# Kernel optimization log

Hardware: AMD Instinct MI355X
Metric: run time of the kernel (lower is better)

Reference implementation:

```python
import jax, jax.numpy as jnp
import numpy as np

B, C, H, W = 8, 256, 64, 64
NUM_HEADS = 4


def setup_inputs() -> dict:
    key = jax.random.key(0)
    ks = jax.random.split(key, 6)
    s = 0.02  # small init scale for 1x1 conv weights
    return {
        "x": jax.random.normal(ks[0], (B, C, H, W), jnp.float32),
        "cproj": jax.random.normal(ks[1], (B, C, H, W), jnp.float32),
        "wq": jax.random.normal(ks[2], (C, C), jnp.float32) * s,
        "bq": jnp.zeros((C,), jnp.float32),
        "wkv": jax.random.normal(ks[3], (2 * C, C), jnp.float32) * s,
        "bkv": jnp.zeros((2 * C,), jnp.float32),
        "wo": jax.random.normal(ks[4], (C, C), jnp.float32) * s,  # zero_module in torch; random here for a meaningful baseline
        "bo": jnp.zeros((C,), jnp.float32),
    }


def reference(x, cproj, wq, bq, wkv, bkv, wo, bo):
    Bb, Cc, Hh, Ww = x.shape
    N = Hh * Ww
    h = NUM_HEADS
    d = Cc // h
    scale = 1.0 / jnp.sqrt(jnp.sqrt(jnp.asarray(Cc, jnp.float32)))

    xf = x.reshape(Bb, Cc, N)
    cf = cproj.reshape(Bb, Cc, N)

    # 1x1 convs == channel matmuls
    Q = jnp.einsum('oc,bcn->bon', wq, xf) + bq[None, :, None]           # (B,C,N)
    KV = jnp.einsum('oc,bcn->bon', wkv, cf) + bkv[None, :, None]        # (B,2C,N)
    K, V = KV[:, :Cc], KV[:, Cc:]

    # softmax over channel-dim-within-head for q, over spatial N for k
    q = jax.nn.softmax(Q.reshape(Bb, h, d, N) * scale, axis=2).reshape(Bb, Cc, N)
    k = jax.nn.softmax(K.reshape(Bb, h, d, N), axis=3).reshape(Bb, Cc, N)

    # linear-attention: (B,C,C) context, then project back to N — note heads are mixed, per original bmm
    context = jnp.einsum('bcn,bdn->bcd', k, V)
    out = jnp.einsum('bcd,bdn->bcn', context, q)

    out = jnp.einsum('oc,bcn->bon', wo, out) + bo[None, :, None]
    return out.reshape(Bb, Cc, Hh, Ww)
```

## Files before the change

kernel.cpp:

```cpp
#include <hip/hip_runtime.h>

#define B_ 8
#define C_ 256
#define N_ 4096
#define H_ 4
#define KVC_ 512
#define NSPLIT 8

typedef float f32x4 __attribute__((ext_vector_type(4)));
typedef __bf16 bf16x8 __attribute__((ext_vector_type(8)));
typedef unsigned short u16x8 __attribute__((ext_vector_type(8)));
typedef unsigned short u16x4 __attribute__((ext_vector_type(4)));

union BU8 { u16x8 u; bf16x8 b; };

__device__ __forceinline__ unsigned short f2bf(float f) {
  unsigned u = __float_as_uint(f);
  u += 0x7fff + ((u >> 16) & 1);
  return (unsigned short)(u >> 16);
}

__device__ __forceinline__ f32x4 mfma16(bf16x8 a, bf16x8 b, f32x4 c) {
  return __builtin_amdgcn_mfma_f32_16x16x32_bf16(a, b, c, 0, 0, 0);
}

__global__ __launch_bounds__(256) void qproj_softmax(
    const float* __restrict__ wq, const float* __restrict__ x,
    const float* __restrict__ bq, unsigned short* __restrict__ qT) {
  __shared__ unsigned short As[256][40];
  __shared__ unsigned short Bs[32][68];
  __shared__ float bql[C_];
  const int b = blockIdx.z;
  const int n0 = blockIdx.x * 64;
  const int tid = threadIdx.x;
  const int lane = tid & 63, w = tid >> 6;
  const float* xb = x + (size_t)b * C_ * N_;

  bql[tid] = bq[tid];

  f32x4 acc[16];
#pragma unroll
  for (int i = 0; i < 16; i++) acc[i] = (f32x4){0.f, 0.f, 0.f, 0.f};

  const int colL = lane & 15, kq = lane >> 4;
  for (int kc = 0; kc < C_; kc += 32) {
    __syncthreads();
#pragma unroll
    for (int i = 0; i < 8; i++) {
      int r = i * 32 + (tid >> 3), c = (tid & 7) * 4;
      float4 v = *(const float4*)&wq[r * C_ + kc + c];
      *(u16x4*)&As[r][c] = (u16x4){f2bf(v.x), f2bf(v.y), f2bf(v.z), f2bf(v.w)};
    }
#pragma unroll
    for (int i = 0; i < 2; i++) {
      int r = i * 16 + (tid >> 4), c = (tid & 15) * 4;
      float4 v = *(const float4*)&xb[(size_t)(kc + r) * N_ + n0 + c];
      *(u16x4*)&Bs[r][c] = (u16x4){f2bf(v.x), f2bf(v.y), f2bf(v.z), f2bf(v.w)};
    }
    __syncthreads();

    BU8 bu;
#pragma unroll
    for (int j = 0; j < 8; j++) bu.u[j] = Bs[kq * 8 + j][w * 16 + colL];
    bf16x8 bf = bu.b;
#pragma unroll
    for (int mt = 0; mt < 16; mt++) {
      bf16x8 af = *(const bf16x8*)&As[mt * 16 + colL][kq * 8];
      acc[mt] = mfma16(af, bf, acc[mt]);
    }
  }

  const int quad = lane >> 4;
  const int n = n0 + w * 16 + colL;
  unsigned short* qbase = qT + ((size_t)b * N_ + n) * C_;
#pragma unroll
  for (int h = 0; h < H_; h++) {
    float v[16];
    float mx = -1e30f;
#pragma unroll
    for (int i = 0; i < 4; i++) {
      int mt = 4 * h + i;
#pragma unroll
      for (int r = 0; r < 4; r++) {
        int m = mt * 16 + quad * 4 + r;
        float val = (acc[mt][r] + bql[m]) * 0.25f;
        v[i * 4 + r] = val;
        mx = fmaxf(mx, val);
      }
    }
    mx = fmaxf(mx, __shfl_xor(mx, 16));
    mx = fmaxf(mx, __shfl_xor(mx, 32));
    float s = 0.f;
#pragma unroll
    for (int j = 0; j < 16; j++) { v[j] = __expf(v[j] - mx); s += v[j]; }
    s += __shfl_xor(s, 16);
    s += __shfl_xor(s, 32);
    float inv = 1.0f / s;
#pragma unroll
    for (int i = 0; i < 4; i++) {
      u16x4 o = (u16x4){f2bf(v[i * 4 + 0] * inv), f2bf(v[i * 4 + 1] * inv),
                        f2bf(v[i * 4 + 2] * inv), f2bf(v[i * 4 + 3] * inv)};
      *(u16x4*)(qbase + (4 * h + i) * 16 + quad * 4) = o;
    }
  }
}

__global__ __launch_bounds__(256) void kvproj(
    const float* __restrict__ wkv, const float* __restrict__ cp,
    const float* __restrict__ bkv, float* __restrict__ Kf,
    unsigned short* __restrict__ Vb) {
  __shared__ unsigned short As[128][40];
  __shared__ unsigned short Bs[32][136];
  const int b = blockIdx.z;
  const int m0 = blockIdx.y * 128, n0 = blockIdx.x * 128;
  const int tid = threadIdx.x, lane = tid & 63, w = tid >> 6;
  const int m0w = (w >> 1) * 64, n0w = (w & 1) * 64;
  const int colL = lane & 15, kq = lane >> 4;
  const float* cpb = cp + (size_t)b * C_ * N_;

  f32x4 acc[4][4];
#pragma unroll
  for (int i = 0; i < 4; i++)
#pragma unroll
    for (int j = 0; j < 4; j++) acc[i][j] = (f32x4){0.f, 0.f, 0.f, 0.f};

  for (int kc = 0; kc < C_; kc += 32) {
    __syncthreads();
#pragma unroll
    for (int i = 0; i < 4; i++) {
      int r = i * 32 + (tid >> 3), c = (tid & 7) * 4;
      float4 v = *(const float4*)&wkv[(size_t)(m0 + r) * C_ + kc + c];
      *(u16x4*)&As[r][c] = (u16x4){f2bf(v.x), f2bf(v.y), f2bf(v.z), f2bf(v.w)};
    }
#pragma unroll
    for (int i = 0; i < 4; i++) {
      int r = i * 8 + (tid >> 5), c = (tid & 31) * 4;
      float4 v = *(const float4*)&cpb[(size_t)(kc + r) * N_ + n0 + c];
      *(u16x4*)&Bs[r][c] = (u16x4){f2bf(v.x), f2bf(v.y), f2bf(v.z), f2bf(v.w)};
    }
    __syncthreads();

    bf16x8 bfr[4];
#pragma unroll
    for (int nt = 0; nt < 4; nt++) {
      BU8 bu;
#pragma unroll
      for (int j = 0; j < 8; j++) bu.u[j] = Bs[kq * 8 + j][n0w + nt * 16 + colL];
      bfr[nt] = bu.b;
    }
#pragma unroll
    for (int mt = 0; mt < 4; mt++) {
      bf16x8 af = *(const bf16x8*)&As[m0w + mt * 16 + colL][kq * 8];
#pragma unroll
      for (int nt = 0; nt < 4; nt++) acc[mt][nt] = mfma16(af, bfr[nt], acc[mt][nt]);
    }
  }

  const int quad = lane >> 4;
#pragma unroll
  for (int mt = 0; mt < 4; mt++) {
#pragma unroll
    for (int r = 0; r < 4; r++) {
      int m = m0 + m0w + mt * 16 + quad * 4 + r;
      float bias = bkv[m];
#pragma unroll
      for (int nt = 0; nt < 4; nt++) {
        int n = n0 + n0w + nt * 16 + colL;
        float val = acc[mt][nt][r] + bias;
        if (m0 < C_) {
          Kf[((size_t)b * C_ + m) * N_ + n] = val;
        } else {
          Vb[((size_t)b * C_ + (m - C_)) * N_ + n] = f2bf(val);
        }
      }
    }
  }
}

__global__ __launch_bounds__(256) void ksoftmax(const float* __restrict__ Kf,
                                                unsigned short* __restrict__ kb) {
  const int b = blockIdx.x >> 8, c = blockIdx.x & 255;
  const float* row = Kf + ((size_t)b * C_ + c) * N_;
  unsigned short* orow = kb + ((size_t)b * C_ + c) * N_;
  const int t = threadIdx.x, lane = t & 63, wv = t >> 6;
  __shared__ float red[8];

  float4 v[4];
  float mx = -1e30f;
#pragma unroll
  for (int i = 0; i < 4; i++) {
    v[i] = *(const float4*)&row[i * 1024 + t * 4];
    mx = fmaxf(fmaxf(fmaxf(mx, v[i].x), fmaxf(v[i].y, v[i].z)), v[i].w);
  }
#pragma unroll
  for (int o = 32; o > 0; o >>= 1) mx = fmaxf(mx, __shfl_down(mx, o));
  if (lane == 0) red[wv] = mx;
  __syncthreads();
  mx = fmaxf(fmaxf(red[0], red[1]), fmaxf(red[2], red[3]));

  float s = 0.f;
#pragma unroll
  for (int i = 0; i < 4; i++) {
    v[i].x = __expf(v[i].x - mx); v[i].y = __expf(v[i].y - mx);
    v[i].z = __expf(v[i].z - mx); v[i].w = __expf(v[i].w - mx);
    s += v[i].x + v[i].y + v[i].z + v[i].w;
  }
#pragma unroll
  for (int o = 32; o > 0; o >>= 1) s += __shfl_down(s, o);
  if (lane == 0) red[4 + wv] = s;
  __syncthreads();
  float inv = 1.0f / (red[4] + red[5] + red[6] + red[7]);
#pragma unroll
  for (int i = 0; i < 4; i++) {
    u16x4 o = (u16x4){f2bf(v[i].x * inv), f2bf(v[i].y * inv),
                      f2bf(v[i].z * inv), f2bf(v[i].w * inv)};
    *(u16x4*)&orow[i * 1024 + t * 4] = o;
  }
}

__global__ __launch_bounds__(256) void ctx_part(
    const unsigned short* __restrict__ kb, const unsigned short* __restrict__ Vb,
    float* __restrict__ ctxp) {
  __shared__ unsigned short As[128][40];
  __shared__ unsigned short Bs[128][40];
  const int z = blockIdx.z, b = z >> 3, s = z & 7;
  const int m0 = blockIdx.y * 128, n0 = blockIdx.x * 128;
  const int tid = threadIdx.x, lane = tid & 63, w = tid >> 6;
  const int m0w = (w >> 1) * 64, n0w = (w & 1) * 64;
  const int colL = lane & 15, kq = lane >> 4;
  const unsigned short* Ab = kb + (size_t)b * C_ * N_;
  const unsigned short* Bb = Vb + (size_t)b * C_ * N_;

  f32x4 acc[4][4];
#pragma unroll
  for (int i = 0; i < 4; i++)
#pragma unroll
    for (int j = 0; j < 4; j++) acc[i][j] = (f32x4){0.f, 0.f, 0.f, 0.f};

  const int kbeg = s * (N_ / NSPLIT);
  for (int kc = kbeg; kc < kbeg + N_ / NSPLIT; kc += 32) {
    __syncthreads();
#pragma unroll
    for (int i = 0; i < 2; i++) {
      int r = i * 64 + (tid >> 2), c = (tid & 3) * 8;
      *(u16x8*)&As[r][c] = *(const u16x8*)&Ab[(size_t)(m0 + r) * N_ + kc + c];
      *(u16x8*)&Bs[r][c] = *(const u16x8*)&Bb[(size_t)(n0 + r) * N_ + kc + c];
    }
    __syncthreads();

    bf16x8 af[4], bfr[4];
#pragma unroll
    for (int mt = 0; mt < 4; mt++) af[mt] = *(const bf16x8*)&As[m0w + mt * 16 + colL][kq * 8];
#pragma unroll
    for (int nt = 0; nt < 4; nt++) bfr[nt] = *(const bf16x8*)&Bs[n0w + nt * 16 + colL][kq * 8];
#pragma unroll
    for (int mt = 0; mt < 4; mt++)
#pragma unroll
      for (int nt = 0; nt < 4; nt++) acc[mt][nt] = mfma16(af[mt], bfr[nt], acc[mt][nt]);
  }

  float* outp = ctxp + ((size_t)s * B_ + b) * C_ * C_;
  const int quad = lane >> 4;
#pragma unroll
  for (int mt = 0; mt < 4; mt++)
#pragma unroll
    for (int nt = 0; nt < 4; nt++)
#pragma unroll
      for (int r = 0; r < 4; r++) {
        int m = m0 + m0w + mt * 16 + quad * 4 + r;
        int n = n0 + n0w + nt * 16 + colL;
        outp[(size_t)m * C_ + n] = acc[mt][nt][r];
      }
}

__global__ __launch_bounds__(256) void ctx_reduce(const float* __restrict__ ctxp,
                                                  unsigned short* __restrict__ ctxs) {
  const size_t e = ((size_t)blockIdx.x * 256 + threadIdx.x) * 4;
  float4 a = {0.f, 0.f, 0.f, 0.f};
#pragma unroll
  for (int s = 0; s < NSPLIT; s++) {
    float4 v = *(const float4*)&ctxp[(size_t)s * B_ * C_ * C_ + e];
    a.x += v.x; a.y += v.y; a.z += v.z; a.w += v.w;
  }
  *(u16x4*)&ctxs[e] = (u16x4){f2bf(a.x), f2bf(a.y), f2bf(a.z), f2bf(a.w)};
}

__global__ __launch_bounds__(256) void oproj(const float* __restrict__ wo,
                                             const unsigned short* __restrict__ ctxs,
                                             unsigned short* __restrict__ ctx2) {
  __shared__ unsigned short As[128][40];
  __shared__ unsigned short Bs[32][136];
  const int b = blockIdx.z;
  const int m0 = blockIdx.y * 128, n0 = blockIdx.x * 128;
  const int tid = threadIdx.x, lane = tid & 63, w = tid >> 6;
  const int m0w = (w >> 1) * 64, n0w = (w & 1) * 64;
  const int colL = lane & 15, kq = lane >> 4;
  const unsigned short* cb = ctxs + (size_t)b * C_ * C_;

  f32x4 acc[4][4];
#pragma unroll
  for (int i = 0; i < 4; i++)
#pragma unroll
    for (int j = 0; j < 4; j++) acc[i][j] = (f32x4){0.f, 0.f, 0.f, 0.f};

  for (int kc = 0; kc < C_; kc += 32) {
    __syncthreads();
#pragma unroll
    for (int i = 0; i < 4; i++) {
      int r = i * 32 + (tid >> 3), c = (tid & 7) * 4;
      float4 v = *(const float4*)&wo[(size_t)(m0 + r) * C_ + kc + c];
      *(u16x4*)&As[r][c] = (u16x4){f2bf(v.x), f2bf(v.y), f2bf(v.z), f2bf(v.w)};
    }
#pragma unroll
    for (int i = 0; i < 2; i++) {
      int r = i * 16 + (tid >> 4), c = (tid & 15) * 8;
      *(u16x8*)&Bs[r][c] = *(const u16x8*)&cb[(size_t)(kc + r) * C_ + n0 + c];
    }
    __syncthreads();

    bf16x8 bfr[4];
#pragma unroll
    for (int nt = 0; nt < 4; nt++) {
      BU8 bu;
#pragma unroll
      for (int j = 0; j < 8; j++) bu.u[j] = Bs[kq * 8 + j][n0w + nt * 16 + colL];
      bfr[nt] = bu.b;
    }
#pragma unroll
    for (int mt = 0; mt < 4; mt++) {
      bf16x8 af = *(const bf16x8*)&As[m0w + mt * 16 + colL][kq * 8];
#pragma unroll
      for (int nt = 0; nt < 4; nt++) acc[mt][nt] = mfma16(af, bfr[nt], acc[mt][nt]);
    }
  }

  unsigned short* ob = ctx2 + (size_t)b * C_ * C_;
  const int quad = lane >> 4;
#pragma unroll
  for (int mt = 0; mt < 4; mt++)
#pragma unroll
    for (int nt = 0; nt < 4; nt++)
#pragma unroll
      for (int r = 0; r < 4; r++) {
        int m = m0 + m0w + mt * 16 + quad * 4 + r;
        int n = n0 + n0w + nt * 16 + colL;
        ob[(size_t)m * C_ + n] = f2bf(acc[mt][nt][r]);
      }
}

__global__ __launch_bounds__(256) void outgemm(const unsigned short* __restrict__ ctx2,
                                               const unsigned short* __restrict__ qT,
                                               const float* __restrict__ bo,
                                               float* __restrict__ out) {
  __shared__ unsigned short As[128][40];
  __shared__ unsigned short Bs[128][40];
  const int b = blockIdx.z;
  const int n0 = blockIdx.x * 128, m0 = blockIdx.y * 128;
  const int tid = threadIdx.x, lane = tid & 63, w = tid >> 6;
  const int m0w = (w >> 1) * 64, n0w = (w & 1) * 64;
  const int colL = lane & 15, kq = lane >> 4;
  const unsigned short* Ab = ctx2 + (size_t)b * C_ * C_;
  const unsigned short* Bb = qT + (size_t)b * N_ * C_;

  f32x4 acc[4][4];
#pragma unroll
  for (int i = 0; i < 4; i++)
#pragma unroll
    for (int j = 0; j < 4; j++) acc[i][j] = (f32x4){0.f, 0.f, 0.f, 0.f};

  for (int kc = 0; kc < C_; kc += 32) {
    __syncthreads();
#pragma unroll
    for (int i = 0; i < 2; i++) {
      int r = i * 64 + (tid >> 2), c = (tid & 3) * 8;
      *(u16x8*)&As[r][c] = *(const u16x8*)&Ab[(size_t)(m0 + r) * C_ + kc + c];
      *(u16x8*)&Bs[r][c] = *(const u16x8*)&Bb[(size_t)(n0 + r) * C_ + kc + c];
    }
    __syncthreads();

    bf16x8 af[4], bfr[4];
#pragma unroll
    for (int mt = 0; mt < 4; mt++) af[mt] = *(const bf16x8*)&As[m0w + mt * 16 + colL][kq * 8];
#pragma unroll
    for (int nt = 0; nt < 4; nt++) bfr[nt] = *(const bf16x8*)&Bs[n0w + nt * 16 + colL][kq * 8];
#pragma unroll
    for (int mt = 0; mt < 4; mt++)
#pragma unroll
      for (int nt = 0; nt < 4; nt++) acc[mt][nt] = mfma16(af[mt], bfr[nt], acc[mt][nt]);
  }

  float* ob = out + (size_t)b * C_ * N_;
  const int quad = lane >> 4;
#pragma unroll
  for (int mt = 0; mt < 4; mt++)
#pragma unroll
    for (int r = 0; r < 4; r++) {
      int m = m0 + m0w + mt * 16 + quad * 4 + r;
      float bias = bo[m];
#pragma unroll
      for (int nt = 0; nt < 4; nt++) {
        int n = n0 + n0w + nt * 16 + colL;
        ob[(size_t)m * N_ + n] = acc[mt][nt][r] + bias;
      }
    }
}

extern "C" void kernel_launch(void* const* d_in, const int* in_sizes, int n_in,
                              void* d_out, int out_size, void* d_ws, size_t ws_size,
                              hipStream_t stream) {
  const float* x     = (const float*)d_in[0];
  const float* cproj = (const float*)d_in[1];
  const float* wq    = (const float*)d_in[2];
  const float* bq    = (const float*)d_in[3];
  const float* wkv   = (const float*)d_in[4];
  const float* bkv   = (const float*)d_in[5];
  const float* wo    = (const float*)d_in[6];
  const float* bo    = (const float*)d_in[7];
  float* out = (float*)d_out;

  unsigned short* qT   = (unsigned short*)d_ws;
  float*          Kf   = (float*)(qT + (size_t)B_ * N_ * C_);
  unsigned short* Vb   = (unsigned short*)(Kf + (size_t)B_ * C_ * N_);
  unsigned short* kb   = Vb + (size_t)B_ * C_ * N_;
  float*          ctxp = (float*)(kb + (size_t)B_ * C_ * N_);
  unsigned short* ctxs = (unsigned short*)(ctxp + (size_t)NSPLIT * B_ * C_ * C_);
  unsigned short* ctx2 = ctxs + (size_t)B_ * C_ * C_;

  qproj_softmax<<<dim3(N_ / 64, 1, B_), 256, 0, stream>>>(wq, x, bq, qT);
  kvproj<<<dim3(N_ / 128, KVC_ / 128, B_), 256, 0, stream>>>(wkv, cproj, bkv, Kf, Vb);
  ksoftmax<<<dim3(B_ * C_), 256, 0, stream>>>(Kf, kb);
  ctx_part<<<dim3(2, 2, B_ * NSPLIT), 256, 0, stream>>>(kb, Vb, ctxp);
  ctx_reduce<<<dim3(B_ * C_ * C_ / 1024), 256, 0, stream>>>(ctxp, ctxs);
  oproj<<<dim3(2, 2, B_), 256, 0, stream>>>(wo, ctxs, ctx2);
  outgemm<<<dim3(N_ / 128, 2, B_), 256, 0, stream>>>(ctx2, qT, bo, out);
}
```

Measured before the change: 216.8 us.

## Register-prefetch next K tiles in GEMM kernels and widen K tile to 64

Four GEMM kernels (qgemm, kvgemm, ctx_part, outgemm) now load the next K-slice from global memory into registers while MFMAs run on the current shared-memory tile. This is meant to hide global load latency behind compute. ctx_part and outgemm also widen the shared K tile from 32 to 64, which halves the number of barrier pairs per tile. In exchange the kernels use more registers and LDS, which may lower occupancy.

```diff
diff --git a/kernel.cpp b/kernel.cpp
--- a/kernel.cpp
+++ b/kernel.cpp
@@ -43,22 +43,34 @@
   for (int i = 0; i < 16; i++) acc[i] = (f32x4){0.f, 0.f, 0.f, 0.f};
 
   const int colL = lane & 15, kq = lane >> 4;
-  for (int kc = 0; kc < C_; kc += 32) {
-    __syncthreads();
+  const int ra = tid >> 3, ca = (tid & 7) * 4;
+  const int rb = tid >> 4, cb = (tid & 15) * 4;
+
+  float4 pa[8], pb[2];
+#pragma unroll
+  for (int i = 0; i < 8; i++) pa[i] = *(const float4*)&wq[(i * 32 + ra) * C_ + ca];
+#pragma unroll
+  for (int i = 0; i < 2; i++) pb[i] = *(const float4*)&xb[(size_t)(i * 16 + rb) * N_ + n0 + cb];
+
+  for (int kt = 0; kt < 8; kt++) {
 #pragma unroll
     for (int i = 0; i < 8; i++) {
-      int r = i * 32 + (tid >> 3), c = (tid & 7) * 4;
-      float4 v = *(const float4*)&wq[r * C_ + kc + c];
-      *(u16x4*)&As[r][c] = (u16x4){f2bf(v.x), f2bf(v.y), f2bf(v.z), f2bf(v.w)};
+      float4 v = pa[i];
+      *(u16x4*)&As[i * 32 + ra][ca] = (u16x4){f2bf(v.x), f2bf(v.y), f2bf(v.z), f2bf(v.w)};
     }
 #pragma unroll
     for (int i = 0; i < 2; i++) {
-      int r = i * 16 + (tid >> 4), c = (tid & 15) * 4;
-      float4 v = *(const float4*)&xb[(size_t)(kc + r) * N_ + n0 + c];
-      *(u16x4*)&Bs[r][c] = (u16x4){f2bf(v.x), f2bf(v.y), f2bf(v.z), f2bf(v.w)};
-    }
-    __syncthreads();
-
+      float4 v = pb[i];
+      *(u16x4*)&Bs[i * 16 + rb][cb] = (u16x4){f2bf(v.x), f2bf(v.y), f2bf(v.z), f2bf(v.w)};
+    }
+    __syncthreads();
+    if (kt < 7) {
+      const int kc = (kt + 1) * 32;
+#pragma unroll
+      for (int i = 0; i < 8; i++) pa[i] = *(const float4*)&wq[(i * 32 + ra) * C_ + kc + ca];
+#pragma unroll
+      for (int i = 0; i < 2; i++) pb[i] = *(const float4*)&xb[(size_t)(kc + i * 16 + rb) * N_ + n0 + cb];
+    }
     BU8 bu;
 #pragma unroll
     for (int j = 0; j < 8; j++) bu.u[j] = Bs[kq * 8 + j][w * 16 + colL];
@@ -68,6 +80,7 @@
       bf16x8 af = *(const bf16x8*)&As[mt * 16 + colL][kq * 8];
       acc[mt] = mfma16(af, bf, acc[mt]);
     }
+    __syncthreads();
   }
 
   const int quad = lane >> 4;
@@ -124,22 +137,34 @@
 #pragma unroll
     for (int j = 0; j < 4; j++) acc[i][j] = (f32x4){0.f, 0.f, 0.f, 0.f};
 
-  for (int kc = 0; kc < C_; kc += 32) {
-    __syncthreads();
-#pragma unroll
-    for (int i = 0; i < 4; i++) {
-      int r = i * 32 + (tid >> 3), c = (tid & 7) * 4;
-      float4 v = *(const float4*)&wkv[(size_t)(m0 + r) * C_ + kc + c];
-      *(u16x4*)&As[r][c] = (u16x4){f2bf(v.x), f2bf(v.y), f2bf(v.z), f2bf(v.w)};
-    }
-#pragma unroll
-    for (int i = 0; i < 4; i++) {
-      int r = i * 8 + (tid >> 5), c = (tid & 31) * 4;
-      float4 v = *(const float4*)&cpb[(size_t)(kc + r) * N_ + n0 + c];
-      *(u16x4*)&Bs[r][c] = (u16x4){f2bf(v.x), f2bf(v.y), f2bf(v.z), f2bf(v.w)};
-    }
-    __syncthreads();
-
+  const int ra = tid >> 3, ca = (tid & 7) * 4;
+  const int rb = tid >> 5, cb = (tid & 31) * 4;
+
+  float4 pa[4], pb[4];
+#pragma unroll
+  for (int i = 0; i < 4; i++) pa[i] = *(const float4*)&wkv[(size_t)(m0 + i * 32 + ra) * C_ + ca];
+#pragma unroll
+  for (int i = 0; i < 4; i++) pb[i] = *(const float4*)&cpb[(size_t)(i * 8 + rb) * N_ + n0 + cb];
+
+  for (int kt = 0; kt < 8; kt++) {
+#pragma unroll
+    for (int i = 0; i < 4; i++) {
+      float4 v = pa[i];
+      *(u16x4*)&As[i * 32 + ra][ca] = (u16x4){f2bf(v.x), f2bf(v.y), f2bf(v.z), f2bf(v.w)};
+    }
+#pragma unroll
+    for (int i = 0; i < 4; i++) {
+      float4 v = pb[i];
+      *(u16x4*)&Bs[i * 8 + rb][cb] = (u16x4){f2bf(v.x), f2bf(v.y), f2bf(v.z), f2bf(v.w)};
+    }
+    __syncthreads();
+    if (kt < 7) {
+      const int kc = (kt + 1) * 32;
+#pragma unroll
+      for (int i = 0; i < 4; i++) pa[i] = *(const float4*)&wkv[(size_t)(m0 + i * 32 + ra) * C_ + kc + ca];
+#pragma unroll
+      for (int i = 0; i < 4; i++) pb[i] = *(const float4*)&cpb[(size_t)(kc + i * 8 + rb) * N_ + n0 + cb];
+    }
     bf16x8 bfr[4];
 #pragma unroll
     for (int nt = 0; nt < 4; nt++) {
@@ -154,6 +179,7 @@
 #pragma unroll
       for (int nt = 0; nt < 4; nt++) acc[mt][nt] = mfma16(af, bfr[nt], acc[mt][nt]);
     }
+    __syncthreads();
   }
 
   const int quad = lane >> 4;
@@ -221,8 +247,8 @@
 __global__ __launch_bounds__(256) void ctx_part(
     const unsigned short* __restrict__ kb, const unsigned short* __restrict__ Vb,
     float* __restrict__ ctxp) {
-  __shared__ unsigned short As[128][40];
-  __shared__ unsigned short Bs[128][40];
+  __shared__ unsigned short As[128][72];
+  __shared__ unsigned short Bs[128][72];
   const int z = blockIdx.z, b = z >> 3, s = z & 7;
   const int m0 = blockIdx.y * 128, n0 = blockIdx.x * 128;
   const int tid = threadIdx.x, lane = tid & 63, w = tid >> 6;
@@ -237,26 +263,44 @@
 #pragma unroll
     for (int j = 0; j < 4; j++) acc[i][j] = (f32x4){0.f, 0.f, 0.f, 0.f};
 
+  const int rs = tid >> 3, cs = (tid & 7) * 8;
   const int kbeg = s * (N_ / NSPLIT);
-  for (int kc = kbeg; kc < kbeg + N_ / NSPLIT; kc += 32) {
-    __syncthreads();
-#pragma unroll
-    for (int i = 0; i < 2; i++) {
-      int r = i * 64 + (tid >> 2), c = (tid & 3) * 8;
-      *(u16x8*)&As[r][c] = *(const u16x8*)&Ab[(size_t)(m0 + r) * N_ + kc + c];
-      *(u16x8*)&Bs[r][c] = *(const u16x8*)&Bb[(size_t)(n0 + r) * N_ + kc + c];
-    }
-    __syncthreads();
-
-    bf16x8 af[4], bfr[4];
-#pragma unroll
-    for (int mt = 0; mt < 4; mt++) af[mt] = *(const bf16x8*)&As[m0w + mt * 16 + colL][kq * 8];
-#pragma unroll
-    for (int nt = 0; nt < 4; nt++) bfr[nt] = *(const bf16x8*)&Bs[n0w + nt * 16 + colL][kq * 8];
-#pragma unroll
-    for (int mt = 0; mt < 4; mt++)
-#pragma unroll
-      for (int nt = 0; nt < 4; nt++) acc[mt][nt] = mfma16(af[mt], bfr[nt], acc[mt][nt]);
+
+  u16x8 pa[4], pb[4];
+#pragma unroll
+  for (int i = 0; i < 4; i++) {
+    pa[i] = *(const u16x8*)&Ab[(size_t)(m0 + i * 32 + rs) * N_ + kbeg + cs];
+    pb[i] = *(const u16x8*)&Bb[(size_t)(n0 + i * 32 + rs) * N_ + kbeg + cs];
+  }
+
+  for (int kt = 0; kt < (N_ / NSPLIT) / 64; kt++) {
+#pragma unroll
+    for (int i = 0; i < 4; i++) {
+      *(u16x8*)&As[i * 32 + rs][cs] = pa[i];
+      *(u16x8*)&Bs[i * 32 + rs][cs] = pb[i];
+    }
+    __syncthreads();
+    if (kt < (N_ / NSPLIT) / 64 - 1) {
+      const int kc = kbeg + (kt + 1) * 64;
+#pragma unroll
+      for (int i = 0; i < 4; i++) {
+        pa[i] = *(const u16x8*)&Ab[(size_t)(m0 + i * 32 + rs) * N_ + kc + cs];
+        pb[i] = *(const u16x8*)&Bb[(size_t)(n0 + i * 32 + rs) * N_ + kc + cs];
+      }
+    }
+#pragma unroll
+    for (int ks = 0; ks < 2; ks++) {
+      bf16x8 af[4], bfr[4];
+#pragma unroll
+      for (int mt = 0; mt < 4; mt++) af[mt] = *(const bf16x8*)&As[m0w + mt * 16 + colL][ks * 32 + kq * 8];
+#pragma unroll
+      for (int nt = 0; nt < 4; nt++) bfr[nt] = *(const bf16x8*)&Bs[n0w + nt * 16 + colL][ks * 32 + kq * 8];
+#pragma unroll
+      for (int mt = 0; mt < 4; mt++)
+#pragma unroll
+        for (int nt = 0; nt < 4; nt++) acc[mt][nt] = mfma16(af[mt], bfr[nt], acc[mt][nt]);
+    }
+    __syncthreads();
   }
 
   float* outp = ctxp + ((size_t)s * B_ + b) * C_ * C_;
@@ -352,8 +396,8 @@
                                                const unsigned short* __restrict__ qT,
                                                const float* __restrict__ bo,
                                                float* __restrict__ out) {
-  __shared__ unsigned short As[128][40];
-  __shared__ unsigned short Bs[128][40];
+  __shared__ unsigned short As[128][72];
+  __shared__ unsigned short Bs[128][72];
   const int b = blockIdx.z;
   const int n0 = blockIdx.x * 128, m0 = blockIdx.y * 128;
   const int tid = threadIdx.x, lane = tid & 63, w = tid >> 6;
@@ -368,25 +412,43 @@
 #pragma unroll
     for (int j = 0; j < 4; j++) acc[i][j] = (f32x4){0.f, 0.f, 0.f, 0.f};
 
-  for (int kc = 0; kc < C_; kc += 32) {
-    __syncthreads();
-#pragma unroll
-    for (int i = 0; i < 2; i++) {
-      int r = i * 64 + (tid >> 2), c = (tid & 3) * 8;
-      *(u16x8*)&As[r][c] = *(const u16x8*)&Ab[(size_t)(m0 + r) * C_ + kc + c];
-      *(u16x8*)&Bs[r][c] = *(const u16x8*)&Bb[(size_t)(n0 + r) * C_ + kc + c];
-    }
-    __syncthreads();
-
-    bf16x8 af[4], bfr[4];
-#pragma unroll
-    for (int mt = 0; mt < 4; mt++) af[mt] = *(const bf16x8*)&As[m0w + mt * 16 + colL][kq * 8];
-#pragma unroll
-    for (int nt = 0; nt < 4; nt++) bfr[nt] = *(const bf16x8*)&Bs[n0w + nt * 16 + colL][kq * 8];
-#pragma unroll
-    for (int mt = 0; mt < 4; mt++)
-#pragma unroll
-      for (int nt = 0; nt < 4; nt++) acc[mt][nt] = mfma16(af[mt], bfr[nt], acc[mt][nt]);
+  const int rs = tid >> 3, cs = (tid & 7) * 8;
+
+  u16x8 pa[4], pb[4];
+#pragma unroll
+  for (int i = 0; i < 4; i++) {
+    pa[i] = *(const u16x8*)&Ab[(size_t)(m0 + i * 32 + rs) * C_ + cs];
+    pb[i] = *(const u16x8*)&Bb[(size_t)(n0 + i * 32 + rs) * C_ + cs];
+  }
+
+  for (int kt = 0; kt < 4; kt++) {
+#pragma unroll
+    for (int i = 0; i < 4; i++) {
+      *(u16x8*)&As[i * 32 + rs][cs] = pa[i];
+      *(u16x8*)&Bs[i * 32 + rs][cs] = pb[i];
+    }
+    __syncthreads();
+    if (kt < 3) {
+      const int kc = (kt + 1) * 64;
+#pragma unroll
+      for (int i = 0; i < 4; i++) {
+        pa[i] = *(const u16x8*)&Ab[(size_t)(m0 + i * 32 + rs) * C_ + kc + cs];
+        pb[i] = *(const u16x8*)&Bb[(size_t)(n0 + i * 32 + rs) * C_ + kc + cs];
+      }
+    }
+#pragma unroll
+    for (int ks = 0; ks < 2; ks++) {
+      bf16x8 af[4], bfr[4];
+#pragma unroll
+      for (int mt = 0; mt < 4; mt++) af[mt] = *(const bf16x8*)&As[m0w + mt * 16 + colL][ks * 32 + kq * 8];
+#pragma unroll
+      for (int nt = 0; nt < 4; nt++) bfr[nt] = *(const bf16x8*)&Bs[n0w + nt * 16 + colL][ks * 32 + kq * 8];
+#pragma unroll
+      for (int mt = 0; mt < 4; mt++)
+#pragma unroll
+        for (int nt = 0; nt < 4; nt++) acc[mt][nt] = mfma16(af[mt], bfr[nt], acc[mt][nt]);
+    }
+    __syncthreads();
   }
 
   float* ob = out + (size_t)b * C_ * N_;
```

Result: faster. 207.7 us (-4.2%).
